# Optimization experiments

Measured on AMD Instinct MI355X. Metric: run time of the kernel, lower is better.

## Reference

```python
import jax, jax.numpy as jnp
import numpy as np

SCALE = 2
EPS = 1e-5  # BatchNorm2d default eps


def conv1x1(x, W, b):
    # x: [B,C,H,W], W: [O,C], b: [O]
    return jnp.einsum('bchw,oc->bohw', x, W) + b[None, :, None, None]


def maxpool(x, s):
    B, C, H, W = x.shape
    return x.reshape(B, C, H // s, s, W // s, s).max(axis=(3, 5))


def upsample_bilinear_ac(x, s):
    # bilinear upsample, align_corners=True
    B, C, H, W = x.shape
    Ho, Wo = H * s, W * s
    ys = jnp.arange(Ho) * ((H - 1) / (Ho - 1))
    xs = jnp.arange(Wo) * ((W - 1) / (Wo - 1))
    y0 = jnp.floor(ys).astype(jnp.int32)
    y1 = jnp.minimum(y0 + 1, H - 1)
    wy = (ys - y0).astype(x.dtype)
    x0 = jnp.floor(xs).astype(jnp.int32)
    x1 = jnp.minimum(x0 + 1, W - 1)
    wx = (xs - x0).astype(x.dtype)
    rows = x[:, :, y0, :] * (1 - wy)[None, None, :, None] + x[:, :, y1, :] * wy[None, None, :, None]
    return rows[:, :, :, x0] * (1 - wx) + rows[:, :, :, x1] * wx


def setup_inputs() -> dict:
    key = jax.random.key(0)
    ks = jax.random.split(key, 9)
    B, Cin, Cm, dk, H, W = 4, 64, 64, 64, 128, 128
    return {
        'x': jax.random.normal(ks[0], (B, Cin, H, W), jnp.float32),
        'memory': jax.random.normal(ks[1], (B, Cm, H, W), jnp.float32),
        'W_qkv': jax.random.normal(ks[2], (3 * dk, Cm), jnp.float32) * 0.05,
        'b_qkv': jax.random.normal(ks[3], (3 * dk,), jnp.float32) * 0.05,
        'W_out': jax.random.normal(ks[4], (Cin, dk), jnp.float32) * 0.05,
        'b_out': jax.random.normal(ks[5], (Cin,), jnp.float32) * 0.05,
        'bn_gamma': jax.random.uniform(ks[6], (Cin,), jnp.float32, 0.5, 1.5),
        'bn_beta': jax.random.normal(ks[7], (Cin,), jnp.float32) * 0.05,
        'gamma': jax.random.normal(ks[8], (1,), jnp.float32) * 0.1,
    }


def reference(x, memory, W_qkv, b_qkv, W_out, b_out, bn_gamma, bn_beta, gamma):
    d_k = W_qkv.shape[0] // 3
    qkv = conv1x1(memory, W_qkv, b_qkv)
    qkv = maxpool(qkv, SCALE)
    q, k, v = jnp.split(qkv, 3, axis=1)
    B, C, H, W = v.shape
    q = q.reshape(B, C, H * W).transpose(0, 2, 1)  # [B,N,C]
    k = k.reshape(B, C, H * W)                      # [B,C,N]
    v = v.reshape(B, C, H * W).transpose(0, 2, 1)   # [B,N,C]
    scale = jnp.asarray(d_k, x.dtype) ** 0.5
    attn = jax.nn.softmax(jnp.einsum('bnc,bcm->bnm', q, k) / scale, axis=-1)
    S = jnp.einsum('bnm,bmc->bnc', attn, v).transpose(0, 2, 1).reshape(B, C, H, W)
    S = upsample_bilinear_ac(S, SCALE)
    S = conv1x1(S, W_out, b_out)
    # BatchNorm2d (training mode: biased batch stats over B,H,W)
    mean = S.mean(axis=(0, 2, 3), keepdims=True)
    var = S.var(axis=(0, 2, 3), keepdims=True)
    S = (S - mean) / jnp.sqrt(var + EPS) * bn_gamma[None, :, None, None] + bn_beta[None, :, None, None]
    return x + gamma[0] * S
```

## Files before the change

### kernel.cpp

```cpp
#include <hip/hip_runtime.h>
#include <stdint.h>

typedef unsigned short u16;
typedef unsigned int   u32;
typedef __attribute__((ext_vector_type(8))) __bf16 bf16x8;
typedef __attribute__((ext_vector_type(4))) float  f32x4;
typedef __attribute__((ext_vector_type(2))) float  f32x2;
typedef __attribute__((ext_vector_type(4))) u32    u32x4;
typedef __attribute__((ext_vector_type(2))) u32    u32x2;

#define QSCALE 0.18033688011112042f

__device__ __forceinline__ u16 f2bf(float x) {
  u32 u = __builtin_bit_cast(u32, x);
  u = (u + 0x7FFFu + ((u >> 16) & 1u)) >> 16;
  return (u16)u;
}

__device__ __forceinline__ u32 cvt_pk_bf16(float lo, float hi) {
  u32 r;
  asm("v_cvt_pk_bf16_f32 %0, %1, %2" : "=v"(r) : "v"(lo), "v"(hi));
  return r;
}

__global__ __launch_bounds__(512) void k_qkvpool(
    const float* __restrict__ mem, const float* __restrict__ Wqkv,
    const float* __restrict__ bqkv, const float* __restrict__ Wout,
    u16* __restrict__ Q, u16* __restrict__ K, u16* __restrict__ V,
    float* __restrict__ stats)
{
  const int oy = blockIdx.x, b = blockIdx.y, t = threadIdx.x;
  const int w = t >> 6, l4 = t & 15, lh = (t >> 4) & 3;
  const int wq = w & 3, wp = w >> 2;

  if (oy == 0 && b == 0 && t < 128) stats[t] = 0.f;

  __shared__ __align__(16) u16 lds[49152];
  u16* mlds  = lds;
  u16* wlds  = lds + 16384;
  u16* qlds  = lds + 28672;
  u16* klds  = lds + 32768;
  u16* vldsT = lds + 36864;
  u16* wolds = lds + 40960;
  u16* vplds = lds + 45056;

  float bias[3][4];
  #pragma unroll
  for (int j = 0; j < 3; ++j)
    #pragma unroll
    for (int r = 0; r < 4; ++r) {
      int oc = wq * 48 + 16 * j + lh * 4 + r;
      float bv = bqkv[oc];
      bias[j][r] = (oc < 64) ? bv * QSCALE : bv;
    }

  {
    const float* src = mem + ((size_t)b * 64) * 16384 + 2 * oy * 128;
    #pragma unroll
    for (int i = 0; i < 8; ++i) {
      int g = t + 512 * i;
      int px = g & 255, c0 = (g >> 8) * 4;
      float f0 = src[(size_t)(c0 + 0) * 16384 + px];
      float f1 = src[(size_t)(c0 + 1) * 16384 + px];
      float f2 = src[(size_t)(c0 + 2) * 16384 + px];
      float f3 = src[(size_t)(c0 + 3) * 16384 + px];
      u32x2 pk;
      pk[0] = (u32)f2bf(f0) | ((u32)f2bf(f1) << 16);
      pk[1] = (u32)f2bf(f2) | ((u32)f2bf(f3) << 16);
      *(u32x2*)(mlds + px * 64 + (((c0 * 2) ^ ((px & 7) << 4)) >> 1)) = pk;
    }
  }
  {
    #pragma unroll
    for (int i = 0; i < 6; ++i) {
      int g = t + 512 * i;
      int oc = g >> 4, c0 = (g & 15) * 4;
      f32x4 wv = *(const f32x4*)(Wqkv + oc * 64 + c0);
      u32x2 pk;
      pk[0] = (u32)f2bf(wv[0]) | ((u32)f2bf(wv[1]) << 16);
      pk[1] = (u32)f2bf(wv[2]) | ((u32)f2bf(wv[3]) << 16);
      *(u32x2*)(wlds + oc * 64 + (((c0 * 2) ^ ((oc & 7) << 4)) >> 1)) = pk;
    }
  }
  {
    #pragma unroll
    for (int i = 0; i < 2; ++i) {
      int g = t + 512 * i;
      int oc = g >> 4, c0 = (g & 15) * 4;
      f32x4 wv = *(const f32x4*)(Wout + oc * 64 + c0);
      u32x2 pk;
      pk[0] = (u32)f2bf(wv[0]) | ((u32)f2bf(wv[1]) << 16);
      pk[1] = (u32)f2bf(wv[2]) | ((u32)f2bf(wv[3]) << 16);
      *(u32x2*)(wolds + oc * 64 + (((c0 * 2) ^ ((oc & 7) << 4)) >> 1)) = pk;
    }
  }
  __syncthreads();

  const int sw  = (l4 & 7) << 4;
  const int oF0 = ((lh * 16) ^ sw) >> 1;
  const int oF1 = ((64 + lh * 16) ^ sw) >> 1;
  bf16x8 af[3][2];
  #pragma unroll
  for (int j = 0; j < 3; ++j) {
    const u16* ar = wlds + (wq * 48 + 16 * j + l4) * 64;
    af[j][0] = *(const bf16x8*)(ar + oF0);
    af[j][1] = *(const bf16x8*)(ar + oF1);
  }

  #pragma unroll 2
  for (int tpi = 0; tpi < 4; ++tpi) {
    const int tp = wp * 4 + tpi;
    const u16* br0 = mlds + (16 * tp + l4) * 64;
    const u16* br1 = mlds + (128 + 16 * tp + l4) * 64;
    bf16x8 b00 = *(const bf16x8*)(br0 + oF0);
    bf16x8 b01 = *(const bf16x8*)(br0 + oF1);
    bf16x8 b10 = *(const bf16x8*)(br1 + oF0);
    bf16x8 b11 = *(const bf16x8*)(br1 + oF1);
    const int ox = 8 * tp + (l4 >> 1);
    #pragma unroll
    for (int j = 0; j < 3; ++j) {
      f32x4 a0 = {0, 0, 0, 0}, a1 = {0, 0, 0, 0};
      a0 = __builtin_amdgcn_mfma_f32_16x16x32_bf16(af[j][0], b00, a0, 0, 0, 0);
      a0 = __builtin_amdgcn_mfma_f32_16x16x32_bf16(af[j][1], b01, a0, 0, 0, 0);
      a1 = __builtin_amdgcn_mfma_f32_16x16x32_bf16(af[j][0], b10, a1, 0, 0, 0);
      a1 = __builtin_amdgcn_mfma_f32_16x16x32_bf16(af[j][1], b11, a1, 0, 0, 0);
      const int ocj = wq * 48 + 16 * j;
      const float sc = (ocj < 64) ? QSCALE : 1.0f;
      #pragma unroll
      for (int r = 0; r < 4; ++r) {
        float m = fmaxf(a0[r], a1[r]);
        m = fmaxf(m, __shfl_xor(m, 1, 64));
        u16 val = f2bf(m * sc + bias[j][r]);
        if ((l4 & 1) == 0) {
          int oc = ocj + lh * 4 + r;
          if (ocj < 64)       qlds[ox * 64 + oc]        = val;
          else if (ocj < 128) klds[ox * 64 + (oc - 64)] = val;
          else {
            int vch = oc - 128;
            vldsT[ox * 64 + (((vch * 2) ^ ((ox & 7) << 4)) >> 1)] = val;
          }
        }
      }
    }
  }
  __syncthreads();

  {
    const u16* ar = wolds + (wq * 16 + l4) * 64;
    bf16x8 aw0 = *(const bf16x8*)(ar + oF0);
    bf16x8 aw1 = *(const bf16x8*)(ar + oF1);
    #pragma unroll
    for (int nti = 0; nti < 2; ++nti) {
      const int nt = wp * 2 + nti;
      const u16* brow = vldsT + (nt * 16 + l4) * 64;
      bf16x8 bw0 = *(const bf16x8*)(brow + oF0);
      bf16x8 bw1 = *(const bf16x8*)(brow + oF1);
      f32x4 u = {0, 0, 0, 0};
      u = __builtin_amdgcn_mfma_f32_16x16x32_bf16(aw0, bw0, u, 0, 0, 0);
      u = __builtin_amdgcn_mfma_f32_16x16x32_bf16(aw1, bw1, u, 0, 0, 0);
      #pragma unroll
      for (int r = 0; r < 4; ++r) {
        int oc = wq * 16 + lh * 4 + r;
        vplds[oc * 64 + nt * 16 + l4] = f2bf(u[r]);
      }
    }
  }
  __syncthreads();

  {
    int r = t >> 3, e8 = (t & 7) * 8;
    size_t nb = (size_t)oy * 64;
    *(u32x4*)(Q + ((size_t)b * 4096 + nb + r) * 64 + e8) = *(const u32x4*)(qlds + r * 64 + e8);
    *(u32x4*)(K + ((size_t)b * 4096 + nb + r) * 64 + e8) = *(const u32x4*)(klds + r * 64 + e8);
    *(u32x4*)(V + ((size_t)b * 64 + r) * 4096 + nb + e8) = *(const u32x4*)(vplds + r * 64 + e8);
  }
}

__global__ __launch_bounds__(1024, 4) void k_attn(
    const u16* __restrict__ Q, const u16* __restrict__ K,
    const u16* __restrict__ V, const float* __restrict__ bo,
    float* __restrict__ Sa)
{
  const int bid = blockIdx.x, t = threadIdx.x;
  const int xcd = bid & 7;
  const int b   = xcd >> 1;
  const int qb  = ((bid >> 3) << 1) | (xcd & 1);
  const int w = t >> 6, l4 = t & 15, lh = (t >> 4) & 3;
  const int sgrp = w >> 2, wq = w & 3;

  __shared__ __align__(16) u16 kvbuf[16384 + 18432];

  u16* kt_w = kvbuf + sgrp * 4096;
  u16* vt_w = kvbuf + 16384 + sgrp * 4608;

  const int qrow = qb * 64 + wq * 16 + l4;
  const u16* qp = Q + ((size_t)b * 4096 + qrow) * 64 + lh * 8;
  bf16x8 qa0 = *(const bf16x8*)qp;
  bf16x8 qa1 = *(const bf16x8*)(qp + 32);

  f32x4 ot[4] = {{0,0,0,0},{0,0,0,0},{0,0,0,0},{0,0,0,0}};
  float lr = 0.f;

  const int tl = t & 255;
  const int skr = tl >> 2, skc = tl & 3;
  const u16* kgp = K + ((size_t)b * 4096 + sgrp * 1024 + skr) * 64 + skc * 16;
  const u16* vgp = V + ((size_t)b * 64 + skr) * 4096 + sgrp * 1024 + skc * 16;
  const u32 fbw = (u32)(((skr & 3) | (((skr >> 3) & 1) << 2)) << 4);
  u16* kwp0 = kt_w + skr * 64 + ((((u32)(skc * 32))      ^ fbw) >> 1);
  u16* kwp1 = kt_w + skr * 64 + ((((u32)(skc * 32 + 16)) ^ fbw) >> 1);
  u16* vwp  = vt_w + skr * 72 + skc * 16;

  const int rbase = ((l4 >> 2) << 3) + (l4 & 3);
  const int fbr   = ((l4 & 3) | (((l4 >> 2) & 1) << 2)) << 4;
  const int offL  = ((lh * 16) ^ fbr) >> 1;
  const int offH  = offL ^ 32;

  u32x4 xk0 = *(const u32x4*)kgp;
  u32x4 xk1 = *(const u32x4*)(kgp + 8);
  u32x4 xv0 = *(const u32x4*)vgp;
  u32x4 xv1 = *(const u32x4*)(vgp + 8);
  u32x4 yk0 = *(const u32x4*)(kgp + 4096);
  u32x4 yk1 = *(const u32x4*)(kgp + 4096 + 8);
  u32x4 yv0 = *(const u32x4*)(vgp + 64);
  u32x4 yv1 = *(const u32x4*)(vgp + 64 + 8);

#define ATTN_COMPUTE                                                          \
    _Pragma("unroll")                                                         \
    for (int ss = 0; ss < 2; ++ss) {                                          \
      const u16* kr0 = kt_w + (ss * 32 + rbase) * 64;                         \
      const u16* kr1 = kr0 + 4 * 64;                                          \
      bf16x8 vf0 = *(const bf16x8*)(vt_w + (l4)      * 72 + ss * 32 + lh * 8);\
      bf16x8 vf1 = *(const bf16x8*)(vt_w + (16 + l4) * 72 + ss * 32 + lh * 8);\
      bf16x8 vf2 = *(const bf16x8*)(vt_w + (32 + l4) * 72 + ss * 32 + lh * 8);\
      bf16x8 vf3 = *(const bf16x8*)(vt_w + (48 + l4) * 72 + ss * 32 + lh * 8);\
      bf16x8 k00 = *(const bf16x8*)(kr0 + offL);                              \
      bf16x8 k01 = *(const bf16x8*)(kr0 + offH);                              \
      bf16x8 k10 = *(const bf16x8*)(kr1 + offL);                              \
      bf16x8 k11 = *(const bf16x8*)(kr1 + offH);                              \
      f32x4 s0 = {0, 0, 0, 0}, s1 = {0, 0, 0, 0};                             \
      s0 = __builtin_amdgcn_mfma_f32_16x16x32_bf16(k00, qa0, s0, 0, 0, 0);    \
      s0 = __builtin_amdgcn_mfma_f32_16x16x32_bf16(k01, qa1, s0, 0, 0, 0);    \
      s1 = __builtin_amdgcn_mfma_f32_16x16x32_bf16(k10, qa0, s1, 0, 0, 0);    \
      s1 = __builtin_amdgcn_mfma_f32_16x16x32_bf16(k11, qa1, s1, 0, 0, 0);    \
      float p0[4], p1[4];                                                     \
      _Pragma("unroll")                                                       \
      for (int r = 0; r < 4; ++r) {                                           \
        p0[r] = exp2f(s0[r]);                                                 \
        p1[r] = exp2f(s1[r]);                                                 \
        lr += p0[r] + p1[r];                                                  \
      }                                                                       \
      u32x4 pw;                                                               \
      pw[0] = cvt_pk_bf16(p0[0], p0[1]);                                      \
      pw[1] = cvt_pk_bf16(p0[2], p0[3]);                                      \
      pw[2] = cvt_pk_bf16(p1[0], p1[1]);                                      \
      pw[3] = cvt_pk_bf16(p1[2], p1[3]);                                      \
      bf16x8 pf = __builtin_bit_cast(bf16x8, pw);                             \
      ot[0] = __builtin_amdgcn_mfma_f32_16x16x32_bf16(vf0, pf, ot[0], 0, 0, 0);\
      ot[1] = __builtin_amdgcn_mfma_f32_16x16x32_bf16(vf1, pf, ot[1], 0, 0, 0);\
      ot[2] = __builtin_amdgcn_mfma_f32_16x16x32_bf16(vf2, pf, ot[2], 0, 0, 0);\
      ot[3] = __builtin_amdgcn_mfma_f32_16x16x32_bf16(vf3, pf, ot[3], 0, 0, 0);\
    }

  #pragma unroll 1
  for (int kt2 = 0; kt2 < 8; ++kt2) {
    const int kti = kt2 * 2;
    *(u32x4*)kwp0 = xk0;
    *(u32x4*)kwp1 = xk1;
    *(u32x4*)vwp = xv0;
    *(u32x4*)(vwp + 8) = xv1;
    __syncthreads();
    if (kti + 2 < 16) {
      xk0 = *(const u32x4*)(kgp + (kti + 2) * 4096);
      xk1 = *(const u32x4*)(kgp + (kti + 2) * 4096 + 8);
      xv0 = *(const u32x4*)(vgp + (kti + 2) * 64);
      xv1 = *(const u32x4*)(vgp + (kti + 2) * 64 + 8);
    }
    ATTN_COMPUTE
    __syncthreads();
    *(u32x4*)kwp0 = yk0;
    *(u32x4*)kwp1 = yk1;
    *(u32x4*)vwp = yv0;
    *(u32x4*)(vwp + 8) = yv1;
    __syncthreads();
    if (kti + 3 < 16) {
      yk0 = *(const u32x4*)(kgp + (kti + 3) * 4096);
      yk1 = *(const u32x4*)(kgp + (kti + 3) * 4096 + 8);
      yv0 = *(const u32x4*)(vgp + (kti + 3) * 64);
      yv1 = *(const u32x4*)(vgp + (kti + 3) * 64 + 8);
    }
    ATTN_COMPUTE
    __syncthreads();
  }
#undef ATTN_COMPUTE

  lr += __shfl_xor(lr, 16, 64);
  lr += __shfl_xor(lr, 32, 64);

  float* opb = (float*)kvbuf;
  float* mlb = (float*)(kvbuf + 32768);
  #pragma unroll
  for (int d = 0; d < 4; ++d)
    #pragma unroll
    for (int r = 0; r < 4; ++r)
      opb[w * 1024 + (16 * d + lh * 4 + r) * 16 + l4] = ot[d][r];
  if (lh == 0) mlb[w * 16 + l4] = lr;
  __syncthreads();

  const int ch = t >> 4, q0v = (t & 15) * 4;
  const float bout_c = bo[ch];
  f32x4 res;
  #pragma unroll
  for (int j = 0; j < 4; ++j) {
    int q = q0v + j, wq2 = q >> 4, ql = q & 15;
    float L = mlb[(wq2)*16      + ql] + mlb[(4 + wq2)*16  + ql]
            + mlb[(8 + wq2)*16  + ql] + mlb[(12 + wq2)*16 + ql];
    float O = opb[(wq2)*1024      + ch * 16 + ql]
            + opb[(4 + wq2)*1024  + ch * 16 + ql]
            + opb[(8 + wq2)*1024  + ch * 16 + ql]
            + opb[(12 + wq2)*1024 + ch * 16 + ql];
    res[j] = O / L + bout_c;
  }
  *(f32x4*)(Sa + ((size_t)b * 64 + ch) * 4096 + (size_t)qb * 64 + q0v) = res;
}

__global__ __launch_bounds__(1024) void k_stats(const float* __restrict__ U,
                                                float* __restrict__ stats)
{
  const int c = blockIdx.x & 63, b = blockIdx.x >> 6, t = threadIdx.x;
  __shared__ __align__(16) float up[4096];
  __shared__ float red[32];
  *(f32x4*)&up[t * 4] = *(const f32x4*)(U + ((size_t)b * 64 + c) * 4096 + t * 4);
  __syncthreads();
  const float R = 0.49606299212598425f;
  float sum = 0.f, ssq = 0.f;
  #pragma unroll 4
  for (int i = 0; i < 16; ++i) {
    int px = t + 1024 * i;
    int yo = px >> 7, xo = px & 127;
    float ys = yo * R; int y0 = (int)ys; float wy = ys - y0; int y1 = min(y0 + 1, 63);
    float xs = xo * R; int x0 = (int)xs; float wx = xs - x0; int x1 = min(x0 + 1, 63);
    const float* r0 = up + y0 * 64; const float* r1 = up + y1 * 64;
    float v0 = r0[x0] * (1.f - wx) + r0[x1] * wx;
    float v1 = r1[x0] * (1.f - wx) + r1[x1] * wx;
    float v = v0 * (1.f - wy) + v1 * wy;
    sum += v; ssq += v * v;
  }
  #pragma unroll
  for (int d = 32; d >= 1; d >>= 1) {
    sum += __shfl_down(sum, d, 64);
    ssq += __shfl_down(ssq, d, 64);
  }
  if ((t & 63) == 0) { red[t >> 6] = sum; red[16 + (t >> 6)] = ssq; }
  __syncthreads();
  if (t == 0) {
    float s = 0.f, q = 0.f;
    #pragma unroll
    for (int i = 0; i < 16; ++i) { s += red[i]; q += red[16 + i]; }
    atomicAdd(&stats[c], s);
    atomicAdd(&stats[64 + c], q);
  }
}

__global__ __launch_bounds__(1024) void k_apply(
    const float* __restrict__ U, const float* __restrict__ stats,
    const float* __restrict__ x, const float* __restrict__ bng,
    const float* __restrict__ bnb, const float* __restrict__ gam,
    float* __restrict__ out)
{
  const int c = blockIdx.x & 63, b = blockIdx.x >> 6, t = threadIdx.x;
  __shared__ __align__(16) float up[4096];
  *(f32x4*)&up[t * 4] = *(const f32x4*)(U + ((size_t)b * 64 + c) * 4096 + t * 4);
  __syncthreads();
  const float inv = 1.0f / 65536.0f;
  float mean = stats[c] * inv;
  float var  = stats[64 + c] * inv - mean * mean;
  float rsig = rsqrtf(var + 1e-5f);
  float g = gam[0];
  float A  = g * bng[c] * rsig;
  float Bc = g * (bnb[c] - mean * rsig * bng[c]);
  const float R = 0.49606299212598425f;
  const size_t base = ((size_t)b * 64 + c) * 16384;
  #pragma unroll 4
  for (int i = 0; i < 16; ++i) {
    int px = t + 1024 * i;
    int yo = px >> 7, xo = px & 127;
    float ys = yo * R; int y0 = (int)ys; float wy = ys - y0; int y1 = min(y0 + 1, 63);
    float xs = xo * R; int x0 = (int)xs; float wx = xs - x0; int x1 = min(x0 + 1, 63);
    const float* r0 = up + y0 * 64; const float* r1 = up + y1 * 64;
    float v0 = r0[x0] * (1.f - wx) + r0[x1] * wx;
    float v1 = r1[x0] * (1.f - wx) + r1[x1] * wx;
    float v = v0 * (1.f - wy) + v1 * wy;
    out[base + px] = x[base + px] + v * A + Bc;
  }
}

extern "C" void kernel_launch(void* const* d_in, const int* in_sizes, int n_in,
                              void* d_out, int out_size, void* d_ws, size_t ws_size,
                              hipStream_t stream)
{
  const float* x      = (const float*)d_in[0];
  const float* memory = (const float*)d_in[1];
  const float* Wqkv   = (const float*)d_in[2];
  const float* bqkv   = (const float*)d_in[3];
  const float* Wout   = (const float*)d_in[4];
  const float* bout   = (const float*)d_in[5];
  const float* bng    = (const float*)d_in[6];
  const float* bnb    = (const float*)d_in[7];
  const float* gamma  = (const float*)d_in[8];

  char* ws = (char*)d_ws;
  u16*   Q     = (u16*)(ws + 0);
  u16*   Kk    = (u16*)(ws + (2u << 20));
  u16*   Vt    = (u16*)(ws + (4u << 20));
  float* U     = (float*)(ws + (10u << 20));
  float* stats = (float*)(ws + (14u << 20));
  float* out   = (float*)d_out;

  k_qkvpool<<<dim3(64, 4), 512, 0, stream>>>(memory, Wqkv, bqkv, Wout, Q, Kk, Vt, stats);
  k_attn   <<<256, 1024, 0, stream>>>(Q, Kk, Vt, bout, U);
  k_stats  <<<256, 1024, 0, stream>>>(U, stats);
  k_apply  <<<256, 1024, 0, stream>>>(U, stats, x, bng, bnb, gamma, out);
}
```

Measured before the change: 62.64 us.

## Double-buffer K/V tiles in LDS with one barrier per attention step

Replaces the single shared K/V staging buffer and its two-register-set prefetch with two LDS buffers. The loop now computes on the current buffer while writing the next tile, prefetched from global memory, into the other buffer, so each iteration needs one __syncthreads instead of two. This doubles the LDS footprint of the attention block to about 139 KB. That likely allows only one 1024-thread block per CU instead of two, trading occupancy and latency hiding for fewer barriers.

Measured after the change: 61.89 us. About the same (-1.2%).

```diff
diff --git a/kernel.cpp b/kernel.cpp
--- a/kernel.cpp
+++ b/kernel.cpp
@@ -188,10 +188,10 @@
   const int w = t >> 6, l4 = t & 15, lh = (t >> 4) & 3;
   const int sgrp = w >> 2, wq = w & 3;
 
-  __shared__ __align__(16) u16 kvbuf[16384 + 18432];
-
-  u16* kt_w = kvbuf + sgrp * 4096;
-  u16* vt_w = kvbuf + 16384 + sgrp * 4608;
+  __shared__ __align__(16) u16 kvbuf[69632];
+
+  const int kgrp_off = sgrp * 4096;
+  const int vgrp_off = 16384 + sgrp * 4608;
 
   const int qrow = qb * 64 + wq * 16 + l4;
   const u16* qp = Q + ((size_t)b * 4096 + qrow) * 64 + lh * 8;
@@ -206,37 +206,28 @@
   const u16* kgp = K + ((size_t)b * 4096 + sgrp * 1024 + skr) * 64 + skc * 16;
   const u16* vgp = V + ((size_t)b * 64 + skr) * 4096 + sgrp * 1024 + skc * 16;
   const u32 fbw = (u32)(((skr & 3) | (((skr >> 3) & 1) << 2)) << 4);
-  u16* kwp0 = kt_w + skr * 64 + ((((u32)(skc * 32))      ^ fbw) >> 1);
-  u16* kwp1 = kt_w + skr * 64 + ((((u32)(skc * 32 + 16)) ^ fbw) >> 1);
-  u16* vwp  = vt_w + skr * 72 + skc * 16;
+  const u32 kw0 = (u32)(kgrp_off + skr * 64) + ((((u32)(skc * 32))      ^ fbw) >> 1);
+  const u32 kw1 = (u32)(kgrp_off + skr * 64) + ((((u32)(skc * 32 + 16)) ^ fbw) >> 1);
+  const u32 vw  = (u32)(vgrp_off + skr * 72 + skc * 16);
 
   const int rbase = ((l4 >> 2) << 3) + (l4 & 3);
   const int fbr   = ((l4 & 3) | (((l4 >> 2) & 1) << 2)) << 4;
   const int offL  = ((lh * 16) ^ fbr) >> 1;
   const int offH  = offL ^ 32;
 
-  u32x4 xk0 = *(const u32x4*)kgp;
-  u32x4 xk1 = *(const u32x4*)(kgp + 8);
-  u32x4 xv0 = *(const u32x4*)vgp;
-  u32x4 xv1 = *(const u32x4*)(vgp + 8);
-  u32x4 yk0 = *(const u32x4*)(kgp + 4096);
-  u32x4 yk1 = *(const u32x4*)(kgp + 4096 + 8);
-  u32x4 yv0 = *(const u32x4*)(vgp + 64);
-  u32x4 yv1 = *(const u32x4*)(vgp + 64 + 8);
-
-#define ATTN_COMPUTE                                                          \
+#define ATTN_COMPUTE(BB)                                                      \
     _Pragma("unroll")                                                         \
     for (int ss = 0; ss < 2; ++ss) {                                          \
-      const u16* kr0 = kt_w + (ss * 32 + rbase) * 64;                         \
-      const u16* kr1 = kr0 + 4 * 64;                                          \
-      bf16x8 vf0 = *(const bf16x8*)(vt_w + (l4)      * 72 + ss * 32 + lh * 8);\
-      bf16x8 vf1 = *(const bf16x8*)(vt_w + (16 + l4) * 72 + ss * 32 + lh * 8);\
-      bf16x8 vf2 = *(const bf16x8*)(vt_w + (32 + l4) * 72 + ss * 32 + lh * 8);\
-      bf16x8 vf3 = *(const bf16x8*)(vt_w + (48 + l4) * 72 + ss * 32 + lh * 8);\
-      bf16x8 k00 = *(const bf16x8*)(kr0 + offL);                              \
-      bf16x8 k01 = *(const bf16x8*)(kr0 + offH);                              \
-      bf16x8 k10 = *(const bf16x8*)(kr1 + offL);                              \
-      bf16x8 k11 = *(const bf16x8*)(kr1 + offH);                              \
+      const u16* kbase = (BB) + kgrp_off + (ss * 32 + rbase) * 64;            \
+      const u16* vbase = (BB) + vgrp_off + ss * 32 + lh * 8;                  \
+      bf16x8 vf0 = *(const bf16x8*)(vbase + (l4)      * 72);                  \
+      bf16x8 vf1 = *(const bf16x8*)(vbase + (16 + l4) * 72);                  \
+      bf16x8 vf2 = *(const bf16x8*)(vbase + (32 + l4) * 72);                  \
+      bf16x8 vf3 = *(const bf16x8*)(vbase + (48 + l4) * 72);                  \
+      bf16x8 k00 = *(const bf16x8*)(kbase + offL);                            \
+      bf16x8 k01 = *(const bf16x8*)(kbase + offH);                            \
+      bf16x8 k10 = *(const bf16x8*)(kbase + 256 + offL);                      \
+      bf16x8 k11 = *(const bf16x8*)(kbase + 256 + offH);                      \
       f32x4 s0 = {0, 0, 0, 0}, s1 = {0, 0, 0, 0};                             \
       s0 = __builtin_amdgcn_mfma_f32_16x16x32_bf16(k00, qa0, s0, 0, 0, 0);    \
       s0 = __builtin_amdgcn_mfma_f32_16x16x32_bf16(k01, qa1, s0, 0, 0, 0);    \
@@ -261,34 +252,36 @@
       ot[3] = __builtin_amdgcn_mfma_f32_16x16x32_bf16(vf3, pf, ot[3], 0, 0, 0);\
     }
 
-  #pragma unroll 1
-  for (int kt2 = 0; kt2 < 8; ++kt2) {
-    const int kti = kt2 * 2;
-    *(u32x4*)kwp0 = xk0;
-    *(u32x4*)kwp1 = xk1;
-    *(u32x4*)vwp = xv0;
-    *(u32x4*)(vwp + 8) = xv1;
-    __syncthreads();
-    if (kti + 2 < 16) {
-      xk0 = *(const u32x4*)(kgp + (kti + 2) * 4096);
-      xk1 = *(const u32x4*)(kgp + (kti + 2) * 4096 + 8);
-      xv0 = *(const u32x4*)(vgp + (kti + 2) * 64);
-      xv1 = *(const u32x4*)(vgp + (kti + 2) * 64 + 8);
-    }
-    ATTN_COMPUTE
-    __syncthreads();
-    *(u32x4*)kwp0 = yk0;
-    *(u32x4*)kwp1 = yk1;
-    *(u32x4*)vwp = yv0;
-    *(u32x4*)(vwp + 8) = yv1;
-    __syncthreads();
-    if (kti + 3 < 16) {
-      yk0 = *(const u32x4*)(kgp + (kti + 3) * 4096);
-      yk1 = *(const u32x4*)(kgp + (kti + 3) * 4096 + 8);
-      yv0 = *(const u32x4*)(vgp + (kti + 3) * 64);
-      yv1 = *(const u32x4*)(vgp + (kti + 3) * 64 + 8);
-    }
-    ATTN_COMPUTE
+  {
+    u32x4 rk0 = *(const u32x4*)kgp;
+    u32x4 rk1 = *(const u32x4*)(kgp + 8);
+    u32x4 rv0 = *(const u32x4*)vgp;
+    u32x4 rv1 = *(const u32x4*)(vgp + 8);
+    *(u32x4*)(kvbuf + kw0) = rk0;
+    *(u32x4*)(kvbuf + kw1) = rk1;
+    *(u32x4*)(kvbuf + vw)  = rv0;
+    *(u32x4*)(kvbuf + vw + 8) = rv1;
+  }
+  __syncthreads();
+
+  #pragma unroll 2
+  for (int kti = 0; kti < 16; ++kti) {
+    u16* bufc = kvbuf + (kti & 1) * 34816;
+    u16* bufn = kvbuf + ((kti + 1) & 1) * 34816;
+    u32x4 rk0, rk1, rv0, rv1;
+    if (kti + 1 < 16) {
+      rk0 = *(const u32x4*)(kgp + (kti + 1) * 4096);
+      rk1 = *(const u32x4*)(kgp + (kti + 1) * 4096 + 8);
+      rv0 = *(const u32x4*)(vgp + (kti + 1) * 64);
+      rv1 = *(const u32x4*)(vgp + (kti + 1) * 64 + 8);
+    }
+    ATTN_COMPUTE(bufc)
+    if (kti + 1 < 16) {
+      *(u32x4*)(bufn + kw0) = rk0;
+      *(u32x4*)(bufn + kw1) = rk1;
+      *(u32x4*)(bufn + vw)  = rv0;
+      *(u32x4*)(bufn + vw + 8) = rv1;
+    }
     __syncthreads();
   }
 #undef ATTN_COMPUTE
```
